# Kernel tuning notes

Measured on AMD Instinct MI355X. Metric: run time of the kernel, lower is better.

## Reference

```python
import jax, jax.numpy as jnp
import numpy as np

V, E, H = 39, 512, 256  # vocab, emb_size, hidden_size (hard-coded in VQVAE)
B, T = 512, 128


def _p(key, shape, scale=0.05):
    return scale * jax.random.normal(key, shape, dtype=jnp.float32)


def setup_inputs() -> dict:
    key = jax.random.key(0)
    ks = jax.random.split(key, 24)
    inp = {}
    inp["input"] = jax.random.randint(ks[0], (B, T), 0, V)
    inp["src_emb_table"] = _p(ks[1], (V, E))
    inp["trg_emb_table"] = _p(ks[2], (V, E))
    # encoder bidirectional GRU (input E, hidden H), PyTorch layout (3H, in)/(3H, H)
    inp["enc_Wih_f"] = _p(ks[3], (3 * H, E)); inp["enc_Whh_f"] = _p(ks[4], (3 * H, H))
    inp["enc_bih_f"] = _p(ks[5], (3 * H,)); inp["enc_bhh_f"] = _p(ks[6], (3 * H,))
    inp["enc_Wih_b"] = _p(ks[7], (3 * H, E)); inp["enc_Whh_b"] = _p(ks[8], (3 * H, H))
    inp["enc_bih_b"] = _p(ks[9], (3 * H,)); inp["enc_bhh_b"] = _p(ks[10], (3 * H,))
    # bridge: Linear(2H -> H, bias=True)
    inp["bridge_W"] = _p(ks[11], (H, 2 * H)); inp["bridge_b"] = _p(ks[12], (H,))
    # Bahdanau attention: key (2H->H), query (H->H), energy (H->1), all bias-free
    inp["attn_Wk"] = _p(ks[13], (H, 2 * H))
    inp["attn_Wq"] = _p(ks[14], (H, H))
    inp["attn_We"] = _p(ks[15], (1, H))
    # decoder GRU (input E + 2H = 1024, hidden H)
    inp["dec_Wih"] = _p(ks[16], (3 * H, E + 2 * H)); inp["dec_Whh"] = _p(ks[17], (3 * H, H))
    inp["dec_bih"] = _p(ks[18], (3 * H,)); inp["dec_bhh"] = _p(ks[19], (3 * H,))
    # pre_output: Linear(H + 2H + E = 1280 -> H, bias=False)
    inp["pre_W"] = _p(ks[20], (H, H + 2 * H + E))
    # generator: Linear(H -> V, bias=False)
    inp["gen_W"] = _p(ks[21], (V, H))
    return inp


def gru_cell(x, h, Wih, Whh, bih, bhh):
    """PyTorch GRU cell: gates ordered [r, z, n]."""
    gi = x @ Wih.T + bih
    gh = h @ Whh.T + bhh
    ir, iz, inn = jnp.split(gi, 3, axis=-1)
    hr, hz, hn = jnp.split(gh, 3, axis=-1)
    r = jax.nn.sigmoid(ir + hr)
    z = jax.nn.sigmoid(iz + hz)
    n = jnp.tanh(inn + r * hn)
    return (1.0 - z) * n + z * h


def reference(input, src_emb_table, trg_emb_table,
              enc_Wih_f, enc_Whh_f, enc_bih_f, enc_bhh_f,
              enc_Wih_b, enc_Whh_b, enc_bih_b, enc_bhh_b,
              bridge_W, bridge_b, attn_Wk, attn_Wq, attn_We,
              dec_Wih, dec_Whh, dec_bih, dec_bhh, pre_W, gen_W):
    Bv, Tv = input.shape
    src_mask = input != 0                       # (B, T)
    trg = input[:, :-1]
    trg_y = input[:, 1:]

    # ---- Encoder: bidirectional GRU over full length (lengths == T) ----
    x = src_emb_table[input]                    # (B, T, E)
    xs = jnp.swapaxes(x, 0, 1)                  # (T, B, E)
    h0 = jnp.zeros((Bv, H), x.dtype)

    def step_f(h, xt):
        hn = gru_cell(xt, h, enc_Wih_f, enc_Whh_f, enc_bih_f, enc_bhh_f)
        return hn, hn

    def step_b(h, xt):
        hn = gru_cell(xt, h, enc_Wih_b, enc_Whh_b, enc_bih_b, enc_bhh_b)
        return hn, hn

    hf, out_f = jax.lax.scan(step_f, h0, xs)
    hb, out_b = jax.lax.scan(step_b, h0, xs[::-1])
    out_b = out_b[::-1]
    enc_out = jnp.swapaxes(jnp.concatenate([out_f, out_b], -1), 0, 1)  # (B, T, 2H)
    enc_final = jnp.concatenate([hf, hb], -1)                          # (B, 2H)

    # ---- Decoder init + precomputed attention keys ----
    hidden = jnp.tanh(enc_final @ bridge_W.T + bridge_b)               # (B, H)
    proj_key = enc_out @ attn_Wk.T                                     # (B, T, H)

    te = jnp.swapaxes(trg_emb_table[trg], 0, 1)                        # (T-1, B, E)
    neg = jnp.finfo(x.dtype).min

    def dec_step(h, prev_embed):
        q = h @ attn_Wq.T                                              # (B, H)
        e = jnp.tanh(q[:, None, :] + proj_key) @ attn_We[0]            # (B, T)
        e = jnp.where(src_mask, e, neg)
        a = jax.nn.softmax(e, axis=-1)                                 # (B, T)
        ctx = jnp.einsum('bt,btd->bd', a, enc_out)                     # (B, 2H)
        hn = gru_cell(jnp.concatenate([prev_embed, ctx], -1), h,
                      dec_Wih, dec_Whh, dec_bih, dec_bhh)              # (B, H)
        # dropout p=0.2 is identity in eval mode
        pre = jnp.concatenate([prev_embed, hn, ctx], -1) @ pre_W.T     # (B, H)
        return hn, pre

    _, pres = jax.lax.scan(dec_step, hidden, te)                       # (T-1, B, H)

    # ---- Generator + NLL loss (sum, ignore_index=0) ----
    logp = jax.nn.log_softmax(pres @ gen_W.T, axis=-1)                 # (T-1, B, V)
    ty = jnp.swapaxes(trg_y, 0, 1)                                     # (T-1, B)
    nll = -jnp.take_along_axis(logp, ty[..., None], axis=-1)[..., 0]
    loss = jnp.sum(jnp.where(ty != 0, nll, 0.0))
    return loss
```

## Files before the change

### kernel.cpp

```cpp
#include <hip/hip_runtime.h>

#define BB 512
#define TT 128
#define EE 512
#define HH 256
#define VV 39
#define H3 768
#define H2 512
#define TM1 127
#define NEGF (-3.402823466e38f)

typedef unsigned short u16;
typedef unsigned char u8;
typedef unsigned int u32;
typedef __attribute__((ext_vector_type(8))) short s16x8;
typedef __attribute__((ext_vector_type(4))) float f32x4;
typedef __attribute__((ext_vector_type(2))) unsigned int u32x2;
typedef __attribute__((ext_vector_type(4))) unsigned int u32x4;

__device__ __forceinline__ float b2f(u16 u){ u32 x=((u32)u)<<16; return __uint_as_float(x); }
__device__ __forceinline__ u16 f2b(float f){ u32 x=__float_as_uint(f); u32 r=(x+0x7fffu+((x>>16)&1u))>>16; return (u16)r; }
__device__ __forceinline__ float sigm(float x){ return 1.f/(1.f+__expf(-x)); }
__device__ __forceinline__ float tanh1(float x){ float t=__expf(2.f*x); return 1.f-2.f/(t+1.f); }
__device__ __forceinline__ float bfl(u32 u){ return __uint_as_float(u<<16); }
__device__ __forceinline__ float bfh(u32 u){ return __uint_as_float(u & 0xffff0000u); }
__device__ __forceinline__ float f8f(u32 x){
  u32 m = x & 0x7Fu;
  u32 h = ((x & 0x80u) << 8) | (m ? ((m<<4) + 0x3C00u) : 0u);
  return __uint_as_float(h << 16);
}
__device__ __forceinline__ u8 f2f8(float f){
  u32 b = __float_as_uint(f);
  u32 s = (b>>31)<<7;
  u32 mag = b & 0x7fffffffu;
  if (mag < 0x3C800000u) return (u8)s;
  u32 r = mag + 0x7FFFFu + ((mag>>20)&1u);
  if (r >= 0x43E80000u) return (u8)(s | 0x7Eu);
  u32 E = (r>>23) - 120u; u32 M = (r>>20)&7u;
  return (u8)(s | (E<<3) | M);
}

#define MFMA __builtin_amdgcn_mfma_f32_16x16x32_bf16

__device__ __forceinline__ u32 aload(const u32* p){
  return __hip_atomic_load(p, __ATOMIC_RELAXED, __HIP_MEMORY_SCOPE_AGENT);
}
__device__ __forceinline__ void astore(u32* p, u32 v){
  __hip_atomic_store(p, v, __ATOMIC_RELAXED, __HIP_MEMORY_SCOPE_AGENT);
}
#define QF(g) ((g)*16)

__global__ __launch_bounds__(256) void k_tables(
    const float* __restrict__ src_emb, const float* __restrict__ trg_emb,
    const float* __restrict__ Wih_f, const float* __restrict__ bih_f,
    const float* __restrict__ Wih_b, const float* __restrict__ bih_b,
    const float* __restrict__ dec_Wih, const float* __restrict__ dec_bih,
    const float* __restrict__ pre_W,
    float* __restrict__ tab_gi_f, float* __restrict__ tab_gi_b,
    float* __restrict__ tab_dec, float* __restrict__ tab_pre)
{
  int v = blockIdx.x;
  int y = blockIdx.y;
  int tid = threadIdx.x;
  if (y < 9){
    int seg = y/3, part = y%3;
    int n = part*256 + tid;
    const float* emb; const float* W; const float* bias; float* out; int ldw;
    if (seg==0){ emb=src_emb; W=Wih_f; bias=bih_f; out=tab_gi_f; ldw=EE; }
    else if (seg==1){ emb=src_emb; W=Wih_b; bias=bih_b; out=tab_gi_b; ldw=EE; }
    else { emb=trg_emb; W=dec_Wih; bias=dec_bih; out=tab_dec; ldw=EE+H2; }
    float acc = bias[n];
    const float* er = emb + (size_t)v*EE;
    const float* wr = W + (size_t)n*ldw;
    for (int k=0;k<EE;k++) acc += er[k]*wr[k];
    out[(size_t)v*H3 + n] = acc;
  } else {
    int n = tid;
    float acc = 0.f;
    const float* er = trg_emb + (size_t)v*EE;
    const float* wr = pre_W + (size_t)n*1280;
    for (int k=0;k<EE;k++) acc += er[k]*wr[k];
    tab_pre[(size_t)v*HH + n] = acc;
  }
}

__global__ __launch_bounds__(256) void k_cvt_all(
    const float* __restrict__ eWhh_f, const float* __restrict__ eWhh_b,
    const float* __restrict__ dWhh, const float* __restrict__ dWih,
    const float* __restrict__ Wk, const float* __restrict__ Wq,
    u16* __restrict__ o1, u16* __restrict__ o2, u16* __restrict__ o3,
    u16* __restrict__ o4, u16* __restrict__ o5, u16* __restrict__ o6)
{
  int idx = blockIdx.x*256 + threadIdx.x;
  const float* src; u16* dst; int cols, ld, off, rel;
  if      (idx <  196608){ rel=idx;          src=eWhh_f; dst=o1; cols=256; ld=256;  off=0;   }
  else if (idx <  393216){ rel=idx-196608;   src=eWhh_b; dst=o2; cols=256; ld=256;  off=0;   }
  else if (idx <  589824){ rel=idx-393216;   src=dWhh;   dst=o3; cols=256; ld=256;  off=0;   }
  else if (idx <  983040){ rel=idx-589824;   src=dWih;   dst=o4; cols=512; ld=1024; off=512; }
  else if (idx < 1114112){ rel=idx-983040;   src=Wk;     dst=o5; cols=512; ld=512;  off=0;   }
  else if (idx < 1179648){ rel=idx-1114112;  src=Wq;     dst=o6; cols=256; ld=256;  off=0;   }
  else return;
  int r = rel/cols, c2 = rel - r*cols;
  dst[rel] = f2b(src[(size_t)r*ld + off + c2]);
}

__global__ __launch_bounds__(256) void k_w2(const float* __restrict__ genW,
    const float* __restrict__ preW, u16* __restrict__ w2)
{
  int idx = blockIdx.x*256 + threadIdx.x;
  if (idx >= 64*512) return;
  int v = idx>>9, k = idx&511;
  float acc = 0.f;
  if (v < VV){
    for (int n=0;n<HH;n++) acc += genW[(size_t)v*HH+n]*preW[(size_t)n*1280+768+k];
  }
  w2[idx] = f2b(acc);
}
__global__ __launch_bounds__(256) void k_w3(const float* __restrict__ genW,
    const float* __restrict__ preW, u16* __restrict__ w3)
{
  int idx = blockIdx.x*256 + threadIdx.x;
  if (idx >= 64*256) return;
  int v = idx>>8, k = idx&255;
  float acc = 0.f;
  if (v < VV){
    for (int n=0;n<HH;n++) acc += genW[(size_t)v*HH+n]*preW[(size_t)n*1280+512+k];
  }
  w3[idx] = f2b(acc);
}
__global__ __launch_bounds__(256) void k_tlg(const float* __restrict__ tab_pre,
    const float* __restrict__ genW, float* __restrict__ tlg)
{
  int v1 = blockIdx.x, tid = threadIdx.x;
  if (tid < 64){
    float acc = 0.f;
    if (tid < VV){
      for (int n=0;n<HH;n++) acc += tab_pre[(size_t)v1*HH+n]*genW[(size_t)tid*HH+n];
    }
    tlg[(size_t)v1*64 + tid] = acc;
  }
}

__global__ __launch_bounds__(512) void k_enc_all(const int* __restrict__ input,
    const u16* __restrict__ wb_f, const u16* __restrict__ wb_b,
    const float* __restrict__ bhh_f, const float* __restrict__ bhh_b,
    const float* __restrict__ tab_f, const float* __restrict__ tab_b,
    float* __restrict__ h_f, float* __restrict__ h_b, u16* __restrict__ enc_out)
{
  __shared__ float gh[4][772];
  __shared__ u16 hs[16][264];
  int bx = blockIdx.x;
  int dirb = bx>>7, mt = bx&127;
  int m0 = mt*4;
  int tid = threadIdx.x;
  const float* tab = dirb? tab_b : tab_f;
  const float* bhh = dirb? bhh_b : bhh_f;
  const u16* Wb = dirb? wb_b : wb_f;
  int c = tid & 255, rh = tid>>8;
  float b_r=bhh[c], b_z=bhh[c+256], b_n=bhh[c+512];
  float hreg[2];
  hreg[0]=0.f; hreg[1]=0.f;
  int wv = tid>>6, lane = tid&63, l15 = lane&15, kg=(lane>>4)*8;
  int n0w = wv*96;
  float* hOut = dirb? h_b : h_f;
  { u16* z = &hs[0][0]; for (int e=tid; e<16*264; e+=512) z[e]=0; }
  __syncthreads();

  for (int s=1; s<=TT; s++){
    int tcol = dirb? (TT-s) : (s-1);
    #pragma unroll
    for (int r=0;r<2;r++){
      int row = rh*2 + r;
      int b = m0 + row;
      int tok = input[b*TT + tcol];
      const float* tg = tab + (size_t)tok*H3;
      float g0=0.f, g1=0.f, g2=0.f;
      if (s>1){ g0=gh[row][c]; g1=gh[row][c+256]; g2=gh[row][c+512]; }
      float rg = sigm(tg[c]     + g0 + b_r);
      float zg = sigm(tg[c+256] + g1 + b_z);
      float ng = tanh1(tg[c+512] + rg*(g2 + b_n));
      float hv = (1.f-zg)*ng + zg*hreg[r];
      hreg[r] = hv;
      u16 hb = f2b(hv);
      hs[row][c] = hb;
      enc_out[((size_t)b*TT + tcol)*H2 + (size_t)dirb*HH + c] = hb;
    }
    if (s==TT){
      #pragma unroll
      for (int r=0;r<2;r++)
        hOut[(size_t)(m0+rh*2+r)*HH + c] = hreg[r];
      break;
    }
    __syncthreads();
    f32x4 acc[6];
    #pragma unroll
    for (int nt=0;nt<6;nt++) acc[nt]=(f32x4){0.f,0.f,0.f,0.f};
    const u16* ar0 = &hs[l15][0];
    s16x8 bcur[6], bnext[6];
    #pragma unroll
    for (int nt=0;nt<6;nt++)
      bcur[nt] = *(const s16x8*)(Wb + (size_t)(n0w+nt*16+l15)*HH + kg);
    #pragma unroll
    for (int ko=0;ko<256;ko+=32){
      if (ko<224){
        #pragma unroll
        for (int nt=0;nt<6;nt++)
          bnext[nt] = *(const s16x8*)(Wb + (size_t)(n0w+nt*16+l15)*HH + ko+32 + kg);
      }
      s16x8 a0 = *(const s16x8*)(ar0 + ko + kg);
      #pragma unroll
      for (int nt=0;nt<6;nt++)
        acc[nt] = MFMA(a0, bcur[nt], acc[nt], 0,0,0);
      #pragma unroll
      for (int nt=0;nt<6;nt++) bcur[nt]=bnext[nt];
    }
    int q4 = (lane>>4)*4;
    if (q4 == 0){
      #pragma unroll
      for (int nt=0;nt<6;nt++){
        int col = n0w + nt*16 + l15;
        #pragma unroll
        for (int j=0;j<4;j++)
          gh[j][col] = acc[nt][j];
      }
    }
    __syncthreads();
  }
}

__global__ __launch_bounds__(256) void k_proj(const u16* __restrict__ enc,
    const u16* __restrict__ W, u16* __restrict__ out, int nTot)
{
  int m0 = blockIdx.x*64;
  int tid = threadIdx.x, wv = tid>>6, lane = tid&63;
  int l15 = lane&15, kg = (lane>>4)*8;
  int n0 = blockIdx.y*256 + wv*64;
  f32x4 acc[4][4];
  #pragma unroll
  for (int rt=0;rt<4;rt++)
    #pragma unroll
    for (int nt=0;nt<4;nt++) acc[rt][nt] = (f32x4){0.f,0.f,0.f,0.f};
  for (int ko=0; ko<512; ko+=32){
    s16x8 a[4], b[4];
    #pragma unroll
    for (int rt=0;rt<4;rt++) a[rt] = *(const s16x8*)(enc + (size_t)(m0+rt*16+l15)*H2 + ko + kg);
    #pragma unroll
    for (int nt=0;nt<4;nt++) b[nt] = *(const s16x8*)(W + (size_t)(n0+nt*16+l15)*H2 + ko + kg);
    #pragma unroll
    for (int rt=0;rt<4;rt++)
      #pragma unroll
      for (int nt=0;nt<4;nt++)
        acc[rt][nt] = MFMA(a[rt], b[nt], acc[rt][nt], 0,0,0);
  }
  #pragma unroll
  for (int rt=0;rt<4;rt++){
    int rbase = m0 + rt*16 + (lane>>4)*4;
    #pragma unroll
    for (int nt=0;nt<4;nt++){
      int col = n0 + nt*16 + l15;
      #pragma unroll
      for (int j=0;j<4;j++)
        out[(size_t)(rbase+j)*nTot + col] = f2b(acc[rt][nt][j]);
    }
  }
}

__global__ __launch_bounds__(256) void k_proj_f8(const u16* __restrict__ enc,
    const u16* __restrict__ W, u8* __restrict__ out, int nTot)
{
  int m0 = blockIdx.x*64;
  int tid = threadIdx.x, wv = tid>>6, lane = tid&63;
  int l15 = lane&15, kg = (lane>>4)*8;
  int n0 = blockIdx.y*256 + wv*64;
  f32x4 acc[4][4];
  #pragma unroll
  for (int rt=0;rt<4;rt++)
    #pragma unroll
    for (int nt=0;nt<4;nt++) acc[rt][nt] = (f32x4){0.f,0.f,0.f,0.f};
  for (int ko=0; ko<512; ko+=32){
    s16x8 a[4], b[4];
    #pragma unroll
    for (int rt=0;rt<4;rt++) a[rt] = *(const s16x8*)(enc + (size_t)(m0+rt*16+l15)*H2 + ko + kg);
    #pragma unroll
    for (int nt=0;nt<4;nt++) b[nt] = *(const s16x8*)(W + (size_t)(n0+nt*16+l15)*H2 + ko + kg);
    #pragma unroll
    for (int rt=0;rt<4;rt++)
      #pragma unroll
      for (int nt=0;nt<4;nt++)
        acc[rt][nt] = MFMA(a[rt], b[nt], acc[rt][nt], 0,0,0);
  }
  #pragma unroll
  for (int rt=0;rt<4;rt++){
    int rbase = m0 + rt*16 + (lane>>4)*4;
    #pragma unroll
    for (int nt=0;nt<4;nt++){
      int col = n0 + nt*16 + l15;
      #pragma unroll
      for (int j=0;j<4;j++)
        out[(size_t)(rbase+j)*nTot + col] = f2f8(acc[rt][nt][j]);
    }
  }
}

__global__ __launch_bounds__(256) void k_proj64(const u16* __restrict__ enc,
    const u16* __restrict__ W2, u16* __restrict__ out)
{
  int m0 = blockIdx.x*64;
  int tid = threadIdx.x, wv = tid>>6, lane = tid&63;
  int l15 = lane&15, kg = (lane>>4)*8;
  int n0 = wv*16;
  f32x4 acc[4];
  #pragma unroll
  for (int rt=0;rt<4;rt++) acc[rt] = (f32x4){0.f,0.f,0.f,0.f};
  for (int ko=0; ko<512; ko+=32){
    s16x8 b = *(const s16x8*)(W2 + (size_t)(n0+l15)*H2 + ko + kg);
    #pragma unroll
    for (int rt=0;rt<4;rt++){
      s16x8 a = *(const s16x8*)(enc + (size_t)(m0+rt*16+l15)*H2 + ko + kg);
      acc[rt] = MFMA(a, b, acc[rt], 0,0,0);
    }
  }
  #pragma unroll
  for (int rt=0;rt<4;rt++){
    int rbase = m0 + rt*16 + (lane>>4)*4;
    int col = n0 + l15;
    #pragma unroll
    for (int j=0;j<4;j++)
      out[(size_t)(rbase+j)*64 + col] = f2b(acc[rt][j]);
  }
}

__global__ __launch_bounds__(256) void k_bridge(const float* __restrict__ h_f,
    const float* __restrict__ h_b, const float* __restrict__ bw,
    const float* __restrict__ bb, float* __restrict__ hst)
{
  __shared__ float As[32][68];
  __shared__ float Ws[32][68];
  int n0=blockIdx.x*64, m0=blockIdx.y*64, tid=threadIdx.x;
  int ar=tid>>2, ak=(tid&3)*8;
  int rt=tid>>4, ct=tid&15;
  float acc[4][4];
  #pragma unroll
  for (int j=0;j<4;j++){
    #pragma unroll
    for (int l=0;l<4;l++) acc[j][l]=0.f;
  }
  for (int ko=0;ko<512;ko+=32){
    int k0=ko+ak;
    const float* asrc = (k0<256)? (h_f + (size_t)(m0+ar)*HH + k0)
                                : (h_b + (size_t)(m0+ar)*HH + (k0-256));
    float4 a0=*(const float4*)asrc, a1=*(const float4*)(asrc+4);
    const float* wsrc = bw + (size_t)(n0+ar)*H2 + k0;
    float4 w0=*(const float4*)wsrc, w1=*(const float4*)(wsrc+4);
    __syncthreads();
    As[ak+0][ar]=a0.x; As[ak+1][ar]=a0.y; As[ak+2][ar]=a0.z; As[ak+3][ar]=a0.w;
    As[ak+4][ar]=a1.x; As[ak+5][ar]=a1.y; As[ak+6][ar]=a1.z; As[ak+7][ar]=a1.w;
    Ws[ak+0][ar]=w0.x; Ws[ak+1][ar]=w0.y; Ws[ak+2][ar]=w0.z; Ws[ak+3][ar]=w0.w;
    Ws[ak+4][ar]=w1.x; Ws[ak+5][ar]=w1.y; Ws[ak+6][ar]=w1.z; Ws[ak+7][ar]=w1.w;
    __syncthreads();
    #pragma unroll
    for (int kk=0;kk<32;kk++){
      float4 a=*(const float4*)&As[kk][rt*4];
      float4 w=*(const float4*)&Ws[kk][ct*4];
      float a4[4]={a.x,a.y,a.z,a.w};
      float w4[4]={w.x,w.y,w.z,w.w};
      #pragma unroll
      for (int j=0;j<4;j++){
        #pragma unroll
        for (int l=0;l<4;l++) acc[j][l]+=a4[j]*w4[l];
      }
    }
  }
  #pragma unroll
  for (int j=0;j<4;j++){
    int row=m0+rt*4+j;
    #pragma unroll
    for (int l=0;l<4;l++){
      int col=n0+ct*4+l;
      hst[(size_t)row*HH+col]=tanh1(acc[j][l]+bb[col]);
    }
  }
}

__global__ __launch_bounds__(256) void k_boot(
    const float* __restrict__ hst, const u16* __restrict__ whh,
    const u16* __restrict__ wq, float* __restrict__ ghg,
    float* __restrict__ qg, float* __restrict__ nll)
{
  __shared__ u16 hsb[16][264];
  int bx=blockIdx.x, tid=threadIdx.x;
  int wv=tid>>6, lane=tid&63, l15=lane&15, kg=(lane>>4)*8;
  int b0=bx*16;
  {
    int c=tid;
    for (int r=0;r<16;r++) hsb[r][c] = f2b(hst[(size_t)(b0+r)*HH + c]);
  }
  if (tid<16) nll[b0+tid] = 0.f;
  __syncthreads();
  int rr = (lane>>4)*4;
  for (int nt=0;nt<12;nt++){
    int n0 = wv*192 + nt*16;
    f32x4 acc = (f32x4){0.f,0.f,0.f,0.f};
    for (int ko=0;ko<256;ko+=32){
      s16x8 a = *(const s16x8*)&hsb[l15][ko+kg];
      s16x8 bf = *(const s16x8*)(whh + (size_t)(n0+l15)*HH + ko + kg);
      acc = MFMA(a, bf, acc, 0,0,0);
    }
    #pragma unroll
    for (int jr=0;jr<4;jr++)
      ghg[(size_t)(b0+rr+jr)*H3 + n0 + l15] = acc[jr];
  }
  #pragma unroll
  for (int nt=0;nt<4;nt++){
    int n0 = wv*64 + nt*16;
    f32x4 acc = (f32x4){0.f,0.f,0.f,0.f};
    for (int ko=0;ko<256;ko+=32){
      s16x8 a = *(const s16x8*)&hsb[l15][ko+kg];
      s16x8 bf = *(const s16x8*)(wq + (size_t)(n0+l15)*HH + ko + kg);
      acc = MFMA(a, bf, acc, 0,0,0);
    }
    #pragma unroll
    for (int jr=0;jr<4;jr++)
      qg[(size_t)(b0+rr+jr)*HH + n0 + l15] = acc[jr];
  }
}

__global__ __launch_bounds__(512,4) void k_step(int L,
    const int* __restrict__ input,
    const float* __restrict__ tab_dec, const float* __restrict__ tab_lgt,
    const float* __restrict__ bhh, const float* __restrict__ We,
    const u16* __restrict__ whh, const u16* __restrict__ wq,
    const u16* __restrict__ w3,
    const u16* __restrict__ pk, const u8* __restrict__ eih8,
    const u16* __restrict__ e2,
    float* __restrict__ hst, u32* __restrict__ qgu, float* __restrict__ ghg,
    u16* __restrict__ gicW, const u16* __restrict__ gicR,
    u16* __restrict__ lgcW, const u16* __restrict__ lgcR,
    float* __restrict__ nll, u32* __restrict__ fl)
{
  __shared__ __align__(16) char smem[40960];
  u16 (*gicL)[776] = (u16(*)[776])smem;
  u16 (*lgcL)[64]  = (u16(*)[64])(smem+24832);
  u16 (*hsb)[264]  = (u16(*)[264])(smem+26880);
  float (*lgt)[64] = (float(*)[64])(smem+35328);
  int* stokG       = (int*)(smem+39424);
  float* aL  = (float*)smem;
  int* stok  = (int*)(smem+512);
  float* qS  = (float*)(smem+1024);
  float (*pG)[768] = (float(*)[768])(smem+4096);
  float (*pE)[64]  = (float(*)[64])(smem+28672);

  int bx=blockIdx.x, tid=threadIdx.x;
  int wv=tid>>6, lane=tid&63, l15=lane&15, kg=(lane>>4)*8;

  if (bx < 32 && L > 0){
    int s = L-1;
    int b0 = bx*16;
    int rr = (lane>>4)*4;
    float b_r, b_z, b_n;
    { int c=tid&255; b_r=bhh[c]; b_z=bhh[c+256]; b_n=bhh[c+512]; }
    for (int idx=tid; idx<6144; idx+=512){
      int r = idx/384, k = idx - r*384;
      *(u32*)&gicL[r][2*k] = *(const u32*)(gicR + (size_t)(b0+r)*H3 + 2*k);
    }
    { int r=tid>>5, k=tid&31;
      *(u32*)&lgcL[r][2*k] = *(const u32*)(lgcR + (size_t)(b0+r)*64 + 2*k); }
    if (tid<16) stokG[tid] = input[(b0+tid)*TT + s];
    __syncthreads();
    {
      int c = tid&255, rh = tid>>8;
      for (int r=rh*8; r<rh*8+8; r++){
        int bb = b0+r;
        const float* tg = tab_dec + (size_t)stokG[r]*H3;
        const float* gr = ghg + (size_t)bb*H3;
        float rg = sigm(tg[c]     + b2f(gicL[r][c])     + gr[c]     + b_r);
        float zg = sigm(tg[c+256] + b2f(gicL[r][c+256]) + gr[c+256] + b_z);
        float ng = tanh1(tg[c+512] + b2f(gicL[r][c+512]) + rg*(gr[c+512] + b_n));
        float hv = (1.f-zg)*ng + zg*hst[(size_t)bb*HH + c];
        hst[(size_t)bb*HH + c] = hv;
        hsb[r][c] = f2b(hv);
      }
    }
    __syncthreads();
    {
      f32x4 accq[2];
      accq[0]=(f32x4){0.f,0.f,0.f,0.f}; accq[1]=(f32x4){0.f,0.f,0.f,0.f};
      #pragma unroll
      for (int ko=0;ko<256;ko+=32){
        s16x8 bq0 = *(const s16x8*)(wq + (size_t)(wv*32+l15)*HH + ko + kg);
        s16x8 bq1 = *(const s16x8*)(wq + (size_t)(wv*32+16+l15)*HH + ko + kg);
        s16x8 a = *(const s16x8*)&hsb[l15][ko+kg];
        accq[0] = MFMA(a,bq0,accq[0],0,0,0);
        accq[1] = MFMA(a,bq1,accq[1],0,0,0);
      }
      #pragma unroll
      for (int nt=0;nt<2;nt++)
        #pragma unroll
        for (int jr=0;jr<4;jr++)
          astore(qgu + (size_t)(b0+rr+jr)*HH + wv*32+nt*16+l15,
                 __float_as_uint(accq[nt][jr]));
    }
    __syncthreads();
    if (tid==0) astore(&fl[QF(bx)], (u32)L);
    {
      f32x4 acc6[6];
      #pragma unroll
      for (int nt=0;nt<6;nt++) acc6[nt]=(f32x4){0.f,0.f,0.f,0.f};
      #pragma unroll
      for (int ko=0;ko<256;ko+=32){
        s16x8 b6[6];
        #pragma unroll
        for (int nt=0;nt<6;nt++)
          b6[nt] = *(const s16x8*)(whh + (size_t)(wv*96+nt*16+l15)*HH + ko + kg);
        s16x8 a = *(const s16x8*)&hsb[l15][ko+kg];
        #pragma unroll
        for (int nt=0;nt<6;nt++) acc6[nt]=MFMA(a,b6[nt],acc6[nt],0,0,0);
      }
      #pragma unroll
      for (int nt=0;nt<6;nt++)
        #pragma unroll
        for (int jr=0;jr<4;jr++)
          ghg[(size_t)(b0+rr+jr)*H3 + wv*96+nt*16+l15] = acc6[nt][jr];
    }
    if (wv<4){
      int n0 = wv*16;
      f32x4 acc = (f32x4){0.f,0.f,0.f,0.f};
      for (int ko=0;ko<256;ko+=32){
        s16x8 a = *(const s16x8*)&hsb[l15][ko+kg];
        s16x8 bf = *(const s16x8*)(w3 + (size_t)(n0+l15)*HH + ko + kg);
        acc = MFMA(a,bf,acc,0,0,0);
      }
      #pragma unroll
      for (int jr=0;jr<4;jr++){
        int r = rr+jr, col = n0+l15;
        lgt[r][col] = acc[jr] + tab_lgt[(size_t)stokG[r]*64 + col]
                    + b2f(lgcL[r][col]);
      }
    }
    __syncthreads();
    {
      int r = wv*4 + (lane>>4);
      if (r < 16){
        float v0 = lgt[r][l15];
        float v1 = lgt[r][l15+16];
        float v2 = (l15<7)? lgt[r][l15+32] : NEGF;
        float m = fmaxf(fmaxf(v0,v1),v2);
        #pragma unroll
        for (int off=8; off; off>>=1) m = fmaxf(m, __shfl_xor(m,off));
        float pe = __expf(v0-m) + __expf(v1-m) + ((l15<7)? __expf(v2-m) : 0.f);
        #pragma unroll
        for (int off=8; off; off>>=1) pe += __shfl_xor(pe,off);
        if (l15==0){
          int ty = input[(b0+r)*TT + s+1];
          if (ty != 0) nll[b0+r] += m + __logf(pe) - lgt[r][ty];
        }
      }
    }
    __syncthreads();
  }

  if (L < TM1){
    int r2 = bx;
    int g2 = r2>>4;
    int l32 = lane&31;
    if (tid < TT) stok[tid] = input[r2*TT + tid];
    const u16* pkb = pk + (size_t)r2*TT*HH + l32*8;
    s16x8 kv[8];
    #pragma unroll
    for (int it=0; it<8; it++){
      int t = wv*16 + it*2 + (lane>>5);
      kv[it] = *(const s16x8*)(pkb + (size_t)t*HH);
    }
    float4 w0 = *(const float4*)(We + l32*8);
    float4 w1 = *(const float4*)(We + l32*8 + 4);
    __syncthreads();
    if (L > 0){
      if (tid==0){
        while (aload(&fl[QF(g2)]) < (u32)L) __builtin_amdgcn_s_sleep(1);
      }
      __syncthreads();
    }
    if (tid < 256) qS[tid] = __uint_as_float(aload(qgu + (size_t)r2*HH + tid));
    __syncthreads();
    float4 q0 = *(const float4*)&qS[l32*8];
    float4 q1 = *(const float4*)&qS[l32*8 + 4];
    #pragma unroll
    for (int it=0; it<8; it++){
      int t = wv*16 + it*2 + (lane>>5);
      s16x8 k8 = kv[it];
      float sE = tanh1(q0.x + b2f((u16)k8[0]))*w0.x
               + tanh1(q0.y + b2f((u16)k8[1]))*w0.y
               + tanh1(q0.z + b2f((u16)k8[2]))*w0.z
               + tanh1(q0.w + b2f((u16)k8[3]))*w0.w
               + tanh1(q1.x + b2f((u16)k8[4]))*w1.x
               + tanh1(q1.y + b2f((u16)k8[5]))*w1.y
               + tanh1(q1.z + b2f((u16)k8[6]))*w1.z
               + tanh1(q1.w + b2f((u16)k8[7]))*w1.w;
      #pragma unroll
      for (int off=16; off; off>>=1) sE += __shfl_xor(sE, off);
      if (l32==0) aL[t] = stok[t] ? sE : NEGF;
    }
    __syncthreads();
    if (wv==0){
      float v0 = aL[lane], v1 = aL[64+lane];
      float m = fmaxf(v0,v1);
      #pragma unroll
      for (int off=32; off; off>>=1) m = fmaxf(m, __shfl_xor(m,off));
      float p0 = __expf(v0-m), p1 = __expf(v1-m);
      float sS = p0+p1;
      #pragma unroll
      for (int off=32; off; off>>=1) sS += __shfl_xor(sS,off);
      float inv = 1.f/sS;
      aL[lane] = p0*inv; aL[64+lane] = p1*inv;
    }
    __syncthreads();
    {
      float gA[8], gB[4], eA=0.f;
      #pragma unroll
      for (int e=0;e<8;e++) gA[e]=0.f;
      #pragma unroll
      for (int e=0;e<4;e++) gB[e]=0.f;
      const u8* ei = eih8 + (size_t)r2*TT*H3;
      const u16* ee = e2 + (size_t)r2*TT*64;
      int t0 = wv*16;
      #pragma unroll 4
      for (int tt=0; tt<16; tt++){
        int t = t0+tt;
        float a = aL[t];
        u32x2 v0 = *(const u32x2*)(ei + (size_t)t*H3 + lane*8);
        u32 v1 = *(const u32*)(ei + (size_t)t*H3 + 512 + lane*4);
        float ev = b2f(ee[(size_t)t*64 + lane]);
        gA[0]+=a*f8f(v0.x); gA[1]+=a*f8f(v0.x>>8);
        gA[2]+=a*f8f(v0.x>>16); gA[3]+=a*f8f(v0.x>>24);
        gA[4]+=a*f8f(v0.y); gA[5]+=a*f8f(v0.y>>8);
        gA[6]+=a*f8f(v0.y>>16); gA[7]+=a*f8f(v0.y>>24);
        gB[0]+=a*f8f(v1); gB[1]+=a*f8f(v1>>8);
        gB[2]+=a*f8f(v1>>16); gB[3]+=a*f8f(v1>>24);
        eA += a*ev;
      }
      #pragma unroll
      for (int e=0;e<8;e++) pG[wv][lane*8+e] = gA[e];
      #pragma unroll
      for (int e=0;e<4;e++) pG[wv][512+lane*4+e] = gB[e];
      pE[wv][lane] = eA;
    }
    __syncthreads();
    if (tid < 384){
      float lo=0.f, hi=0.f;
      #pragma unroll
      for (int w=0;w<8;w++){ lo += pG[w][2*tid]; hi += pG[w][2*tid+1]; }
      u32 v = (u32)f2b(lo) | ((u32)f2b(hi)<<16);
      *(u32*)&gicW[(size_t)r2*H3 + 2*tid] = v;
    } else if (tid < 416){
      int d = tid-384;
      float lo=0.f, hi=0.f;
      #pragma unroll
      for (int w=0;w<8;w++){ lo += pE[w][2*d]; hi += pE[w][2*d+1]; }
      u32 v = (u32)f2b(lo) | ((u32)f2b(hi)<<16);
      *(u32*)&lgcW[(size_t)r2*64 + 2*d] = v;
    }
  }
}

__global__ __launch_bounds__(256) void k_loss(const float* __restrict__ nll,
                                              float* __restrict__ out)
{
  __shared__ float sm[256];
  int tid=threadIdx.x;
  float s = nll[tid] + nll[tid+256];
  sm[tid]=s; __syncthreads();
  for (int off=128; off; off>>=1){
    if (tid<off) sm[tid]+=sm[tid+off];
    __syncthreads();
  }
  if (tid==0) out[0]=sm[0];
}

extern "C" void kernel_launch(void* const* d_in, const int* in_sizes, int n_in,
                              void* d_out, int out_size, void* d_ws, size_t ws_size,
                              hipStream_t stream)
{
  const int*   input    = (const int*)  d_in[0];
  const float* src_emb  = (const float*)d_in[1];
  const float* trg_emb  = (const float*)d_in[2];
  const float* eWih_f   = (const float*)d_in[3];
  const float* eWhh_f   = (const float*)d_in[4];
  const float* ebih_f   = (const float*)d_in[5];
  const float* ebhh_f   = (const float*)d_in[6];
  const float* eWih_b   = (const float*)d_in[7];
  const float* eWhh_b   = (const float*)d_in[8];
  const float* ebih_b   = (const float*)d_in[9];
  const float* ebhh_b   = (const float*)d_in[10];
  const float* bridge_W = (const float*)d_in[11];
  const float* bridge_b = (const float*)d_in[12];
  const float* attn_Wk  = (const float*)d_in[13];
  const float* attn_Wq  = (const float*)d_in[14];
  const float* attn_We  = (const float*)d_in[15];
  const float* dec_Wih  = (const float*)d_in[16];
  const float* dec_Whh  = (const float*)d_in[17];
  const float* dec_bih  = (const float*)d_in[18];
  const float* dec_bhh  = (const float*)d_in[19];
  const float* pre_W    = (const float*)d_in[20];
  const float* gen_W    = (const float*)d_in[21];

  float* F = (float*)d_ws;
  size_t o=0;
  u32* fl         = (u32*)(F+o); o+=2048;
  float* tab_gi_f = F+o; o+=(size_t)VV*H3;
  float* tab_gi_b = F+o; o+=(size_t)VV*H3;
  float* tab_dec  = F+o; o+=(size_t)VV*H3;
  float* tab_pre  = F+o; o+=(size_t)VV*HH;
  float* tab_lgt  = F+o; o+=(size_t)VV*64;
  float* h_f      = F+o; o+=(size_t)BB*HH;
  float* h_b      = F+o; o+=(size_t)BB*HH;
  float* hst      = F+o; o+=(size_t)BB*HH;
  float* qg       = F+o; o+=(size_t)BB*HH;
  float* ghg      = F+o; o+=(size_t)BB*H3;
  float* nll      = F+o; o+=(size_t)BB;
  u16* U = (u16*)(F+o);
  size_t uo=0;
  u16* enc_out = U+uo; uo+=(size_t)BB*TT*H2;
  u16* pk      = U+uo; uo+=(size_t)BB*TT*HH;
  u16* e2      = U+uo; uo+=(size_t)BB*TT*64;
  u16* gic0    = U+uo; uo+=(size_t)BB*H3;
  u16* gic1    = U+uo; uo+=(size_t)BB*H3;
  u16* lgc0    = U+uo; uo+=(size_t)BB*64;
  u16* lgc1    = U+uo; uo+=(size_t)BB*64;
  u16* wb_ehh_f= U+uo; uo+=(size_t)H3*HH;
  u16* wb_ehh_b= U+uo; uo+=(size_t)H3*HH;
  u16* wb_dhh  = U+uo; uo+=(size_t)H3*HH;
  u16* wb_dih  = U+uo; uo+=(size_t)H3*H2;
  u16* wb_wk   = U+uo; uo+=(size_t)HH*H2;
  u16* wb_wq   = U+uo; uo+=(size_t)HH*HH;
  u16* wb_w2   = U+uo; uo+=(size_t)64*H2;
  u16* wb_w3   = U+uo; uo+=(size_t)64*HH;
  u8* eih8 = (u8*)(U+uo);

  dim3 blk(256,1,1);
  k_tables<<<dim3(VV,10),blk,0,stream>>>(src_emb,trg_emb,eWih_f,ebih_f,eWih_b,ebih_b,
                                         dec_Wih,dec_bih,pre_W,
                                         tab_gi_f,tab_gi_b,tab_dec,tab_pre);
  k_tlg<<<dim3(VV),blk,0,stream>>>(tab_pre,gen_W,tab_lgt);
  k_cvt_all<<<dim3(4608),blk,0,stream>>>(eWhh_f,eWhh_b,dec_Whh,dec_Wih,attn_Wk,attn_Wq,
                                         wb_ehh_f,wb_ehh_b,wb_dhh,wb_dih,wb_wk,wb_wq);
  k_w2<<<dim3(128),blk,0,stream>>>(gen_W,pre_W,wb_w2);
  k_w3<<<dim3(64),blk,0,stream>>>(gen_W,pre_W,wb_w3);
  k_enc_all<<<dim3(256),dim3(512),0,stream>>>(input,wb_ehh_f,wb_ehh_b,ebhh_f,ebhh_b,
                                              tab_gi_f,tab_gi_b,h_f,h_b,enc_out);
  k_proj<<<dim3(1024,1),blk,0,stream>>>(enc_out,wb_wk,pk,HH);
  k_proj_f8<<<dim3(1024,3),blk,0,stream>>>(enc_out,wb_dih,eih8,H3);
  k_proj64<<<dim3(1024),blk,0,stream>>>(enc_out,wb_w2,e2);
  k_bridge<<<dim3(4,8),blk,0,stream>>>(h_f,h_b,bridge_W,bridge_b,hst);
  k_boot<<<dim3(32),blk,0,stream>>>(hst,wb_dhh,wb_wq,ghg,qg,nll);
  hipMemsetAsync(fl, 0, 8192, stream);

  for (int L=0; L<=TM1; L++){
    u16* gw = (L&1)? gic1 : gic0;
    u16* gr = (L&1)? gic0 : gic1;
    u16* lw = (L&1)? lgc1 : lgc0;
    u16* lr = (L&1)? lgc0 : lgc1;
    k_step<<<dim3(512),dim3(512),0,stream>>>(L,input,tab_dec,tab_lgt,dec_bhh,attn_We,
                                             wb_dhh,wb_wq,wb_w3,
                                             pk,eih8,e2,hst,(u32*)qg,ghg,
                                             gw,gr,lw,lr,nll,fl);
  }
  k_loss<<<dim3(1),blk,0,stream>>>(nll,(float*)d_out);
}
```

Baseline: 7.982 ms.

## Fuse per-step decoder launches into one persistent kernel with flag sync

Replaces the 128 per-timestep launches of the decoder step kernel with a single persistent kernel that loops over time internally. Cross-block dependencies are handled with per-row progress flags and relaxed agent-scope atomic loads and stores on the ping-pong context buffers, and the encoder key tile stays in registers across all steps. NLL is accumulated in a register and written once at the end. This removes launch overhead and the reloads at each launch, but it relies on all 512 blocks being co-resident to avoid deadlock, and relaxed atomics give no ordering guarantees for the data published alongside the flags.

```diff
diff --git a/kernel.cpp b/kernel.cpp
--- a/kernel.cpp
+++ b/kernel.cpp
@@ -49,6 +49,7 @@
   __hip_atomic_store(p, v, __ATOMIC_RELAXED, __HIP_MEMORY_SCOPE_AGENT);
 }
 #define QF(g) ((g)*16)
+#define GF(b) (512 + (b)*16)
 
 __global__ __launch_bounds__(256) void k_tables(
     const float* __restrict__ src_emb, const float* __restrict__ trg_emb,
@@ -425,7 +426,7 @@
   }
 }
 
-__global__ __launch_bounds__(512,4) void k_step(int L,
+__global__ __launch_bounds__(512,4) void k_dec_p(
     const int* __restrict__ input,
     const float* __restrict__ tab_dec, const float* __restrict__ tab_lgt,
     const float* __restrict__ bhh, const float* __restrict__ We,
@@ -434,8 +435,8 @@
     const u16* __restrict__ pk, const u8* __restrict__ eih8,
     const u16* __restrict__ e2,
     float* __restrict__ hst, u32* __restrict__ qgu, float* __restrict__ ghg,
-    u16* __restrict__ gicW, const u16* __restrict__ gicR,
-    u16* __restrict__ lgcW, const u16* __restrict__ lgcR,
+    u32* __restrict__ gp0, u32* __restrict__ gp1,
+    u32* __restrict__ lp0, u32* __restrict__ lp1,
     float* __restrict__ nll, u32* __restrict__ fl)
 {
   __shared__ __align__(16) char smem[40960];
@@ -445,220 +446,242 @@
   float (*lgt)[64] = (float(*)[64])(smem+35328);
   int* stokG       = (int*)(smem+39424);
   float* aL  = (float*)smem;
-  int* stok  = (int*)(smem+512);
   float* qS  = (float*)(smem+1024);
   float (*pG)[768] = (float(*)[768])(smem+4096);
   float (*pE)[64]  = (float(*)[64])(smem+28672);
+  __shared__ int stokD[TT];
 
   int bx=blockIdx.x, tid=threadIdx.x;
   int wv=tid>>6, lane=tid&63, l15=lane&15, kg=(lane>>4)*8;
-
-  if (bx < 32 && L > 0){
-    int s = L-1;
-    int b0 = bx*16;
-    int rr = (lane>>4)*4;
-    float b_r, b_z, b_n;
-    { int c=tid&255; b_r=bhh[c]; b_z=bhh[c+256]; b_n=bhh[c+512]; }
-    for (int idx=tid; idx<6144; idx+=512){
-      int r = idx/384, k = idx - r*384;
-      *(u32*)&gicL[r][2*k] = *(const u32*)(gicR + (size_t)(b0+r)*H3 + 2*k);
-    }
-    { int r=tid>>5, k=tid&31;
-      *(u32*)&lgcL[r][2*k] = *(const u32*)(lgcR + (size_t)(b0+r)*64 + 2*k); }
-    if (tid<16) stokG[tid] = input[(b0+tid)*TT + s];
-    __syncthreads();
-    {
-      int c = tid&255, rh = tid>>8;
-      for (int r=rh*8; r<rh*8+8; r++){
-        int bb = b0+r;
-        const float* tg = tab_dec + (size_t)stokG[r]*H3;
-        const float* gr = ghg + (size_t)bb*H3;
-        float rg = sigm(tg[c]     + b2f(gicL[r][c])     + gr[c]     + b_r);
-        float zg = sigm(tg[c+256] + b2f(gicL[r][c+256]) + gr[c+256] + b_z);
-        float ng = tanh1(tg[c+512] + b2f(gicL[r][c+512]) + rg*(gr[c+512] + b_n));
-        float hv = (1.f-zg)*ng + zg*hst[(size_t)bb*HH + c];
-        hst[(size_t)bb*HH + c] = hv;
-        hsb[r][c] = f2b(hv);
-      }
-    }
-    __syncthreads();
-    {
-      f32x4 accq[2];
-      accq[0]=(f32x4){0.f,0.f,0.f,0.f}; accq[1]=(f32x4){0.f,0.f,0.f,0.f};
-      #pragma unroll
-      for (int ko=0;ko<256;ko+=32){
-        s16x8 bq0 = *(const s16x8*)(wq + (size_t)(wv*32+l15)*HH + ko + kg);
-        s16x8 bq1 = *(const s16x8*)(wq + (size_t)(wv*32+16+l15)*HH + ko + kg);
-        s16x8 a = *(const s16x8*)&hsb[l15][ko+kg];
-        accq[0] = MFMA(a,bq0,accq[0],0,0,0);
-        accq[1] = MFMA(a,bq1,accq[1],0,0,0);
-      }
-      #pragma unroll
-      for (int nt=0;nt<2;nt++)
-        #pragma unroll
-        for (int jr=0;jr<4;jr++)
-          astore(qgu + (size_t)(b0+rr+jr)*HH + wv*32+nt*16+l15,
-                 __float_as_uint(accq[nt][jr]));
-    }
-    __syncthreads();
-    if (tid==0) astore(&fl[QF(bx)], (u32)L);
-    {
-      f32x4 acc6[6];
-      #pragma unroll
-      for (int nt=0;nt<6;nt++) acc6[nt]=(f32x4){0.f,0.f,0.f,0.f};
-      #pragma unroll
-      for (int ko=0;ko<256;ko+=32){
-        s16x8 b6[6];
-        #pragma unroll
-        for (int nt=0;nt<6;nt++)
-          b6[nt] = *(const s16x8*)(whh + (size_t)(wv*96+nt*16+l15)*HH + ko + kg);
-        s16x8 a = *(const s16x8*)&hsb[l15][ko+kg];
-        #pragma unroll
-        for (int nt=0;nt<6;nt++) acc6[nt]=MFMA(a,b6[nt],acc6[nt],0,0,0);
-      }
-      #pragma unroll
-      for (int nt=0;nt<6;nt++)
-        #pragma unroll
-        for (int jr=0;jr<4;jr++)
-          ghg[(size_t)(b0+rr+jr)*H3 + wv*96+nt*16+l15] = acc6[nt][jr];
-    }
-    if (wv<4){
-      int n0 = wv*16;
-      f32x4 acc = (f32x4){0.f,0.f,0.f,0.f};
-      for (int ko=0;ko<256;ko+=32){
-        s16x8 a = *(const s16x8*)&hsb[l15][ko+kg];
-        s16x8 bf = *(const s16x8*)(w3 + (size_t)(n0+l15)*HH + ko + kg);
-        acc = MFMA(a,bf,acc,0,0,0);
-      }
-      #pragma unroll
-      for (int jr=0;jr<4;jr++){
-        int r = rr+jr, col = n0+l15;
-        lgt[r][col] = acc[jr] + tab_lgt[(size_t)stokG[r]*64 + col]
-                    + b2f(lgcL[r][col]);
-      }
-    }
-    __syncthreads();
-    {
-      int r = wv*4 + (lane>>4);
-      if (r < 16){
-        float v0 = lgt[r][l15];
-        float v1 = lgt[r][l15+16];
-        float v2 = (l15<7)? lgt[r][l15+32] : NEGF;
-        float m = fmaxf(fmaxf(v0,v1),v2);
-        #pragma unroll
-        for (int off=8; off; off>>=1) m = fmaxf(m, __shfl_xor(m,off));
-        float pe = __expf(v0-m) + __expf(v1-m) + ((l15<7)? __expf(v2-m) : 0.f);
-        #pragma unroll
-        for (int off=8; off; off>>=1) pe += __shfl_xor(pe,off);
-        if (l15==0){
-          int ty = input[(b0+r)*TT + s+1];
-          if (ty != 0) nll[b0+r] += m + __logf(pe) - lgt[r][ty];
-        }
-      }
-    }
-    __syncthreads();
-  }
-
-  if (L < TM1){
-    int r2 = bx;
-    int g2 = r2>>4;
-    int l32 = lane&31;
-    if (tid < TT) stok[tid] = input[r2*TT + tid];
-    const u16* pkb = pk + (size_t)r2*TT*HH + l32*8;
-    s16x8 kv[8];
+  int rr = (lane>>4)*4;
+  int b0 = bx*16;
+  int g2 = bx>>4;
+  int l32 = lane&31;
+  int isg = (bx<32);
+  float b_r, b_z, b_n;
+  { int c=tid&255; b_r=bhh[c]; b_z=bhh[c+256]; b_n=bhh[c+512]; }
+  float4 w0 = *(const float4*)(We + l32*8);
+  float4 w1 = *(const float4*)(We + l32*8 + 4);
+  if (tid < TT) stokD[tid] = input[bx*TT + tid];
+  s16x8 kv[8];
+  {
+    const u16* pkb = pk + (size_t)bx*TT*HH + l32*8;
     #pragma unroll
     for (int it=0; it<8; it++){
       int t = wv*16 + it*2 + (lane>>5);
       kv[it] = *(const s16x8*)(pkb + (size_t)t*HH);
     }
-    float4 w0 = *(const float4*)(We + l32*8);
-    float4 w1 = *(const float4*)(We + l32*8 + 4);
-    __syncthreads();
-    if (L > 0){
-      if (tid==0){
-        while (aload(&fl[QF(g2)]) < (u32)L) __builtin_amdgcn_s_sleep(1);
-      }
-      __syncthreads();
-    }
-    if (tid < 256) qS[tid] = __uint_as_float(aload(qgu + (size_t)r2*HH + tid));
-    __syncthreads();
-    float4 q0 = *(const float4*)&qS[l32*8];
-    float4 q1 = *(const float4*)&qS[l32*8 + 4];
-    #pragma unroll
-    for (int it=0; it<8; it++){
-      int t = wv*16 + it*2 + (lane>>5);
-      s16x8 k8 = kv[it];
-      float sE = tanh1(q0.x + b2f((u16)k8[0]))*w0.x
-               + tanh1(q0.y + b2f((u16)k8[1]))*w0.y
-               + tanh1(q0.z + b2f((u16)k8[2]))*w0.z
-               + tanh1(q0.w + b2f((u16)k8[3]))*w0.w
-               + tanh1(q1.x + b2f((u16)k8[4]))*w1.x
-               + tanh1(q1.y + b2f((u16)k8[5]))*w1.y
-               + tanh1(q1.z + b2f((u16)k8[6]))*w1.z
-               + tanh1(q1.w + b2f((u16)k8[7]))*w1.w;
-      #pragma unroll
-      for (int off=16; off; off>>=1) sE += __shfl_xor(sE, off);
-      if (l32==0) aL[t] = stok[t] ? sE : NEGF;
-    }
-    __syncthreads();
-    if (wv==0){
-      float v0 = aL[lane], v1 = aL[64+lane];
-      float m = fmaxf(v0,v1);
-      #pragma unroll
-      for (int off=32; off; off>>=1) m = fmaxf(m, __shfl_xor(m,off));
-      float p0 = __expf(v0-m), p1 = __expf(v1-m);
-      float sS = p0+p1;
-      #pragma unroll
-      for (int off=32; off; off>>=1) sS += __shfl_xor(sS,off);
-      float inv = 1.f/sS;
-      aL[lane] = p0*inv; aL[64+lane] = p1*inv;
-    }
-    __syncthreads();
-    {
-      float gA[8], gB[4], eA=0.f;
-      #pragma unroll
-      for (int e=0;e<8;e++) gA[e]=0.f;
-      #pragma unroll
-      for (int e=0;e<4;e++) gB[e]=0.f;
-      const u8* ei = eih8 + (size_t)r2*TT*H3;
-      const u16* ee = e2 + (size_t)r2*TT*64;
-      int t0 = wv*16;
-      #pragma unroll 4
-      for (int tt=0; tt<16; tt++){
-        int t = t0+tt;
-        float a = aL[t];
-        u32x2 v0 = *(const u32x2*)(ei + (size_t)t*H3 + lane*8);
-        u32 v1 = *(const u32*)(ei + (size_t)t*H3 + 512 + lane*4);
-        float ev = b2f(ee[(size_t)t*64 + lane]);
-        gA[0]+=a*f8f(v0.x); gA[1]+=a*f8f(v0.x>>8);
-        gA[2]+=a*f8f(v0.x>>16); gA[3]+=a*f8f(v0.x>>24);
-        gA[4]+=a*f8f(v0.y); gA[5]+=a*f8f(v0.y>>8);
-        gA[6]+=a*f8f(v0.y>>16); gA[7]+=a*f8f(v0.y>>24);
-        gB[0]+=a*f8f(v1); gB[1]+=a*f8f(v1>>8);
-        gB[2]+=a*f8f(v1>>16); gB[3]+=a*f8f(v1>>24);
-        eA += a*ev;
-      }
-      #pragma unroll
-      for (int e=0;e<8;e++) pG[wv][lane*8+e] = gA[e];
-      #pragma unroll
-      for (int e=0;e<4;e++) pG[wv][512+lane*4+e] = gB[e];
-      pE[wv][lane] = eA;
-    }
-    __syncthreads();
-    if (tid < 384){
-      float lo=0.f, hi=0.f;
-      #pragma unroll
-      for (int w=0;w<8;w++){ lo += pG[w][2*tid]; hi += pG[w][2*tid+1]; }
-      u32 v = (u32)f2b(lo) | ((u32)f2b(hi)<<16);
-      *(u32*)&gicW[(size_t)r2*H3 + 2*tid] = v;
-    } else if (tid < 416){
-      int d = tid-384;
-      float lo=0.f, hi=0.f;
-      #pragma unroll
-      for (int w=0;w<8;w++){ lo += pE[w][2*d]; hi += pE[w][2*d+1]; }
-      u32 v = (u32)f2b(lo) | ((u32)f2b(hi)<<16);
-      *(u32*)&lgcW[(size_t)r2*64 + 2*d] = v;
-    }
+  }
+  float nlacc = 0.f;
+  __syncthreads();
+
+  for (int L=0; L<=TM1; L++){
+    if (isg && L > 0){
+      int s = L-1;
+      const u32* gpR = (L&1)? gp0 : gp1;
+      const u32* lpR = (L&1)? lp0 : lp1;
+      if (tid<16){
+        while (aload(&fl[GF(b0+tid)]) < (u32)L) __builtin_amdgcn_s_sleep(1);
+      }
+      if (tid<16) stokG[tid] = input[(b0+tid)*TT + s];
+      __syncthreads();
+      for (int idx=tid; idx<6144; idx+=512){
+        int r = idx/384, k = idx - r*384;
+        u32 v = aload(gpR + (size_t)(b0+r)*384 + k);
+        *(u32*)&gicL[r][2*k] = v;
+      }
+      { int r=tid>>5, k=tid&31;
+        u32 v = aload(lpR + (size_t)(b0+r)*32 + k);
+        *(u32*)&lgcL[r][2*k] = v; }
+      __syncthreads();
+      {
+        int c = tid&255, rh = tid>>8;
+        for (int r=rh*8; r<rh*8+8; r++){
+          int bb = b0+r;
+          const float* tg = tab_dec + (size_t)stokG[r]*H3;
+          const float* gr = ghg + (size_t)bb*H3;
+          float rg = sigm(tg[c]     + b2f(gicL[r][c])     + gr[c]     + b_r);
+          float zg = sigm(tg[c+256] + b2f(gicL[r][c+256]) + gr[c+256] + b_z);
+          float ng = tanh1(tg[c+512] + b2f(gicL[r][c+512]) + rg*(gr[c+512] + b_n));
+          float hv = (1.f-zg)*ng + zg*hst[(size_t)bb*HH + c];
+          hst[(size_t)bb*HH + c] = hv;
+          hsb[r][c] = f2b(hv);
+        }
+      }
+      __syncthreads();
+      {
+        f32x4 accq[2];
+        accq[0]=(f32x4){0.f,0.f,0.f,0.f}; accq[1]=(f32x4){0.f,0.f,0.f,0.f};
+        #pragma unroll
+        for (int ko=0;ko<256;ko+=32){
+          s16x8 bq0 = *(const s16x8*)(wq + (size_t)(wv*32+l15)*HH + ko + kg);
+          s16x8 bq1 = *(const s16x8*)(wq + (size_t)(wv*32+16+l15)*HH + ko + kg);
+          s16x8 a = *(const s16x8*)&hsb[l15][ko+kg];
+          accq[0] = MFMA(a,bq0,accq[0],0,0,0);
+          accq[1] = MFMA(a,bq1,accq[1],0,0,0);
+        }
+        #pragma unroll
+        for (int nt=0;nt<2;nt++)
+          #pragma unroll
+          for (int jr=0;jr<4;jr++)
+            astore(qgu + (size_t)(b0+rr+jr)*HH + wv*32+nt*16+l15,
+                   __float_as_uint(accq[nt][jr]));
+      }
+      __syncthreads();
+      if (tid==0) astore(&fl[QF(bx)], (u32)L);
+      {
+        f32x4 acc6[6];
+        #pragma unroll
+        for (int nt=0;nt<6;nt++) acc6[nt]=(f32x4){0.f,0.f,0.f,0.f};
+        #pragma unroll
+        for (int ko=0;ko<256;ko+=32){
+          s16x8 b6[6];
+          #pragma unroll
+          for (int nt=0;nt<6;nt++)
+            b6[nt] = *(const s16x8*)(whh + (size_t)(wv*96+nt*16+l15)*HH + ko + kg);
+          s16x8 a = *(const s16x8*)&hsb[l15][ko+kg];
+          #pragma unroll
+          for (int nt=0;nt<6;nt++) acc6[nt]=MFMA(a,b6[nt],acc6[nt],0,0,0);
+        }
+        #pragma unroll
+        for (int nt=0;nt<6;nt++)
+          #pragma unroll
+          for (int jr=0;jr<4;jr++)
+            ghg[(size_t)(b0+rr+jr)*H3 + wv*96+nt*16+l15] = acc6[nt][jr];
+      }
+      if (wv<4){
+        int n0 = wv*16;
+        f32x4 acc = (f32x4){0.f,0.f,0.f,0.f};
+        for (int ko=0;ko<256;ko+=32){
+          s16x8 a = *(const s16x8*)&hsb[l15][ko+kg];
+          s16x8 bf = *(const s16x8*)(w3 + (size_t)(n0+l15)*HH + ko + kg);
+          acc = MFMA(a,bf,acc,0,0,0);
+        }
+        #pragma unroll
+        for (int jr=0;jr<4;jr++){
+          int r = rr+jr, col = n0+l15;
+          lgt[r][col] = acc[jr] + tab_lgt[(size_t)stokG[r]*64 + col]
+                      + b2f(lgcL[r][col]);
+        }
+      }
+      __syncthreads();
+      {
+        int r = wv*4 + (lane>>4);
+        if (r < 16){
+          float v0 = lgt[r][l15];
+          float v1 = lgt[r][l15+16];
+          float v2 = (l15<7)? lgt[r][l15+32] : NEGF;
+          float m = fmaxf(fmaxf(v0,v1),v2);
+          #pragma unroll
+          for (int off=8; off; off>>=1) m = fmaxf(m, __shfl_xor(m,off));
+          float pe = __expf(v0-m) + __expf(v1-m) + ((l15<7)? __expf(v2-m) : 0.f);
+          #pragma unroll
+          for (int off=8; off; off>>=1) pe += __shfl_xor(pe,off);
+          if (l15==0){
+            int ty = input[(b0+r)*TT + s+1];
+            if (ty != 0) nlacc += m + __logf(pe) - lgt[r][ty];
+          }
+        }
+      }
+      __syncthreads();
+    }
+
+    if (L < TM1){
+      u32* gpW = (L&1)? gp1 : gp0;
+      u32* lpW = (L&1)? lp1 : lp0;
+      if (L > 0){
+        if (tid==0){
+          while (aload(&fl[QF(g2)]) < (u32)L) __builtin_amdgcn_s_sleep(1);
+        }
+        __syncthreads();
+      }
+      if (tid < 256) qS[tid] = __uint_as_float(aload(qgu + (size_t)bx*HH + tid));
+      __syncthreads();
+      float4 q0 = *(const float4*)&qS[l32*8];
+      float4 q1 = *(const float4*)&qS[l32*8 + 4];
+      #pragma unroll
+      for (int it=0; it<8; it++){
+        int t = wv*16 + it*2 + (lane>>5);
+        s16x8 k8 = kv[it];
+        float sE = tanh1(q0.x + b2f((u16)k8[0]))*w0.x
+                 + tanh1(q0.y + b2f((u16)k8[1]))*w0.y
+                 + tanh1(q0.z + b2f((u16)k8[2]))*w0.z
+                 + tanh1(q0.w + b2f((u16)k8[3]))*w0.w
+                 + tanh1(q1.x + b2f((u16)k8[4]))*w1.x
+                 + tanh1(q1.y + b2f((u16)k8[5]))*w1.y
+                 + tanh1(q1.z + b2f((u16)k8[6]))*w1.z
+                 + tanh1(q1.w + b2f((u16)k8[7]))*w1.w;
+        #pragma unroll
+        for (int off=16; off; off>>=1) sE += __shfl_xor(sE, off);
+        if (l32==0) aL[t] = stokD[t] ? sE : NEGF;
+      }
+      __syncthreads();
+      if (wv==0){
+        float v0 = aL[lane], v1 = aL[64+lane];
+        float m = fmaxf(v0,v1);
+        #pragma unroll
+        for (int off=32; off; off>>=1) m = fmaxf(m, __shfl_xor(m,off));
+        float p0 = __expf(v0-m), p1 = __expf(v1-m);
+        float sS = p0+p1;
+        #pragma unroll
+        for (int off=32; off; off>>=1) sS += __shfl_xor(sS,off);
+        float inv = 1.f/sS;
+        aL[lane] = p0*inv; aL[64+lane] = p1*inv;
+      }
+      __syncthreads();
+      {
+        float gA[8], gB[4], eA=0.f;
+        #pragma unroll
+        for (int e=0;e<8;e++) gA[e]=0.f;
+        #pragma unroll
+        for (int e=0;e<4;e++) gB[e]=0.f;
+        const u8* ei = eih8 + (size_t)bx*TT*H3;
+        const u16* ee = e2 + (size_t)bx*TT*64;
+        int t0 = wv*16;
+        #pragma unroll 4
+        for (int tt=0; tt<16; tt++){
+          int t = t0+tt;
+          float a = aL[t];
+          u32x2 v0 = *(const u32x2*)(ei + (size_t)t*H3 + lane*8);
+          u32 v1 = *(const u32*)(ei + (size_t)t*H3 + 512 + lane*4);
+          float ev = b2f(ee[(size_t)t*64 + lane]);
+          gA[0]+=a*f8f(v0.x); gA[1]+=a*f8f(v0.x>>8);
+          gA[2]+=a*f8f(v0.x>>16); gA[3]+=a*f8f(v0.x>>24);
+          gA[4]+=a*f8f(v0.y); gA[5]+=a*f8f(v0.y>>8);
+          gA[6]+=a*f8f(v0.y>>16); gA[7]+=a*f8f(v0.y>>24);
+          gB[0]+=a*f8f(v1); gB[1]+=a*f8f(v1>>8);
+          gB[2]+=a*f8f(v1>>16); gB[3]+=a*f8f(v1>>24);
+          eA += a*ev;
+        }
+        #pragma unroll
+        for (int e=0;e<8;e++) pG[wv][lane*8+e] = gA[e];
+        #pragma unroll
+        for (int e=0;e<4;e++) pG[wv][512+lane*4+e] = gB[e];
+        pE[wv][lane] = eA;
+      }
+      __syncthreads();
+      if (tid < 384){
+        float lo=0.f, hi=0.f;
+        #pragma unroll
+        for (int w=0;w<8;w++){ lo += pG[w][2*tid]; hi += pG[w][2*tid+1]; }
+        u32 v = (u32)f2b(lo) | ((u32)f2b(hi)<<16);
+        astore(gpW + (size_t)bx*384 + tid, v);
+      } else if (tid < 416){
+        int d = tid-384;
+        float lo=0.f, hi=0.f;
+        #pragma unroll
+        for (int w=0;w<8;w++){ lo += pE[w][2*d]; hi += pE[w][2*d+1]; }
+        u32 v = (u32)f2b(lo) | ((u32)f2b(hi)<<16);
+        astore(lpW + (size_t)bx*32 + d, v);
+      }
+      __syncthreads();
+      if (tid==0) astore(&fl[GF(bx)], (u32)(L+1));
+    }
+  }
+
+  if (isg){
+    int r = wv*4 + (lane>>4);
+    if (r < 16 && l15==0) nll[b0+r] = nlacc;
   }
 }
 
@@ -705,7 +728,7 @@
 
   float* F = (float*)d_ws;
   size_t o=0;
-  u32* fl         = (u32*)(F+o); o+=2048;
+  u32* fl         = (u32*)(F+o); o+=16384;
   float* tab_gi_f = F+o; o+=(size_t)VV*H3;
   float* tab_gi_b = F+o; o+=(size_t)VV*H3;
   float* tab_dec  = F+o; o+=(size_t)VV*H3;
@@ -717,15 +740,15 @@
   float* qg       = F+o; o+=(size_t)BB*HH;
   float* ghg      = F+o; o+=(size_t)BB*H3;
   float* nll      = F+o; o+=(size_t)BB;
+  u32* gp0        = (u32*)(F+o); o+=(size_t)BB*384;
+  u32* gp1        = (u32*)(F+o); o+=(size_t)BB*384;
+  u32* lp0        = (u32*)(F+o); o+=(size_t)BB*32;
+  u32* lp1        = (u32*)(F+o); o+=(size_t)BB*32;
   u16* U = (u16*)(F+o);
   size_t uo=0;
   u16* enc_out = U+uo; uo+=(size_t)BB*TT*H2;
   u16* pk      = U+uo; uo+=(size_t)BB*TT*HH;
   u16* e2      = U+uo; uo+=(size_t)BB*TT*64;
-  u16* gic0    = U+uo; uo+=(size_t)BB*H3;
-  u16* gic1    = U+uo; uo+=(size_t)BB*H3;
-  u16* lgc0    = U+uo; uo+=(size_t)BB*64;
-  u16* lgc1    = U+uo; uo+=(size_t)BB*64;
   u16* wb_ehh_f= U+uo; uo+=(size_t)H3*HH;
   u16* wb_ehh_b= U+uo; uo+=(size_t)H3*HH;
   u16* wb_dhh  = U+uo; uo+=(size_t)H3*HH;
@@ -752,17 +775,10 @@
   k_proj64<<<dim3(1024),blk,0,stream>>>(enc_out,wb_w2,e2);
   k_bridge<<<dim3(4,8),blk,0,stream>>>(h_f,h_b,bridge_W,bridge_b,hst);
   k_boot<<<dim3(32),blk,0,stream>>>(hst,wb_dhh,wb_wq,ghg,qg,nll);
-  hipMemsetAsync(fl, 0, 8192, stream);
-
-  for (int L=0; L<=TM1; L++){
-    u16* gw = (L&1)? gic1 : gic0;
-    u16* gr = (L&1)? gic0 : gic1;
-    u16* lw = (L&1)? lgc1 : lgc0;
-    u16* lr = (L&1)? lgc0 : lgc1;
-    k_step<<<dim3(512),dim3(512),0,stream>>>(L,input,tab_dec,tab_lgt,dec_bhh,attn_We,
-                                             wb_dhh,wb_wq,wb_w3,
-                                             pk,eih8,e2,hst,(u32*)qg,ghg,
-                                             gw,gr,lw,lr,nll,fl);
-  }
+  hipMemsetAsync(fl, 0, 65536, stream);
+  k_dec_p<<<dim3(512),dim3(512),0,stream>>>(input,tab_dec,tab_lgt,dec_bhh,attn_We,
+                                            wb_dhh,wb_wq,wb_w3,
+                                            pk,eih8,e2,hst,(u32*)qg,ghg,
+                                            gp0,gp1,lp0,lp1,nll,fl);
   k_loss<<<dim3(1),blk,0,stream>>>(nll,(float*)d_out);
 }
```

After: 11.95 ms. 49.7% more time.
